# Kernel tuning notes

Hardware: AMD Instinct MI355X
Metric: run time of the kernel (lower is better)

The kernel has to match this reference:

```python
import jax, jax.numpy as jnp
import numpy as np
from math import factorial as _fact

# ---- sizes / hyperparams (match init_kwargs) ----
N_NODES, N_EDGES = 8192, 131072
C, H, NRAD, NUM_LAYERS = 64, 64, 8, 2
R_MAX, AVG_NN = 5.0, 16.0
LS = (0, 1, 2)  # irreps degrees carried by node features and edge SH

# ---- real-basis Clebsch-Gordan coefficients (computed once in numpy) ----
def _cg_scalar(j1, m1, j2, m2, j3, m3):
    if m1 + m2 != m3:
        return 0.0
    pre = ((2*j3+1) * _fact(j1+j2-j3) * _fact(j1-j2+j3) * _fact(-j1+j2+j3)
           / _fact(j1+j2+j3+1)) ** 0.5
    pre *= (_fact(j1+m1)*_fact(j1-m1)*_fact(j2+m2)*_fact(j2-m2)
            * _fact(j3+m3)*_fact(j3-m3)) ** 0.5
    s = 0.0
    for k in range(max(0, j2-j3-m1, j1+m2-j3), min(j1+j2-j3, j1-m1, j2+m2)+1):
        s += (-1)**k / (_fact(k)*_fact(j1+j2-j3-k)*_fact(j1-m1-k)
                        * _fact(j2+m2-k)*_fact(j3-j2+m1+k)*_fact(j3-j1-m2+k))
    return pre * s

def _U_real(l):
    # unitary: Y_real = U @ Y_complex, components ordered m=-l..l
    U = np.zeros((2*l+1, 2*l+1), dtype=complex)
    s2 = 2 ** -0.5
    for m in range(-l, l+1):
        if m > 0:
            U[m+l, m+l] = (-1)**m * s2
            U[m+l, -m+l] = s2
        elif m == 0:
            U[l, l] = 1.0
        else:
            U[m+l, m+l] = 1j*s2
            U[m+l, -m+l] = -1j*(-1)**(-m)*s2
    return U

def _real_cg(l1, l2, l3):
    Cc = np.zeros((2*l1+1, 2*l2+1, 2*l3+1))
    for i1, m1 in enumerate(range(-l1, l1+1)):
        for i2, m2 in enumerate(range(-l2, l2+1)):
            m3 = m1 + m2
            if abs(m3) <= l3:
                Cc[i1, i2, m3+l3] = _cg_scalar(l1, m1, l2, m2, l3, m3)
    U1, U2, U3 = _U_real(l1), _U_real(l2), _U_real(l3)
    W = np.einsum('ia,jb,kc,abc->ijk', U1.conj(), U2.conj(), U3, Cc.astype(complex))
    W = W.real if np.linalg.norm(W.real) >= np.linalg.norm(W.imag) else W.imag
    W = W / np.linalg.norm(W) * (2*l3+1) ** 0.5  # component-style normalization
    return jnp.asarray(W, dtype=jnp.float32)

PATHS = [(l1, l2, l3) for l1 in LS for l2 in LS for l3 in LS
         if abs(l1 - l2) <= l3 <= l1 + l2]  # 15 tensor-product paths
CGS = [_real_cg(*p) for p in PATHS]
N_PATHS = len(PATHS)


def _sph(u):
    # real spherical harmonics of unit vectors, l=0,1,2, m=-l..l ordering
    x, y, z = u[:, 0], u[:, 1], u[:, 2]
    sh0 = jnp.ones((u.shape[0], 1), u.dtype)
    sh1 = jnp.sqrt(3.0) * jnp.stack([y, z, x], axis=-1)
    sh2 = jnp.stack([jnp.sqrt(15.0)*x*y, jnp.sqrt(15.0)*y*z,
                     jnp.sqrt(5.0)/2*(3*z*z - 1.0),
                     jnp.sqrt(15.0)*x*z, jnp.sqrt(15.0)/2*(x*x - y*y)], axis=-1)
    return (sh0, sh1, sh2)


def _forward(positions, embed, w_proj, mlp_w1, mlp_b1, mlp_w2, mlp_b2, mlp_w3,
             lin_self, gate_w, gate_b, species, senders, receivers):
    n = positions.shape[0]
    rel = (positions[receivers] - positions[senders]) / R_MAX  # [E,3]
    d = jnp.linalg.norm(rel, axis=-1)                          # [E]
    u = rel / jnp.maximum(d, 1e-6)[:, None]
    sh = _sph(u)
    freqs = jnp.arange(1, NRAD + 1, dtype=positions.dtype)
    xr = jnp.clip(d, 1e-4, 1.0)[:, None]
    basis = jnp.sqrt(2.0) * jnp.sin(freqs * jnp.pi * xr) / xr  # Bessel [E,NRAD]
    cut = 0.5 * (jnp.cos(jnp.pi * jnp.clip(d, 0.0, 1.0)) + 1.0)  # smooth cutoff

    # initial species embedding -> scalar (0e) features; l>0 start at zero
    x0 = embed[species] @ w_proj                                # [N,C]
    feats = [x0[:, :, None],
             jnp.zeros((n, C, 3), x0.dtype),
             jnp.zeros((n, C, 5), x0.dtype)]

    inv_sqrt_nn = 1.0 / jnp.sqrt(jnp.asarray(AVG_NN, x0.dtype))
    for i in range(NUM_LAYERS):
        # radial MLP -> per-path, per-channel edge weights
        h = jax.nn.silu(basis @ mlp_w1[i] + mlp_b1[i])
        h = jax.nn.silu(h @ mlp_w2[i] + mlp_b2[i])
        w = (h @ mlp_w3[i]).reshape(-1, N_PATHS, C) * cut[:, None, None]
        xg = [feats[l][senders] for l in LS]                    # edge gather
        msgs = [0.0, 0.0, 0.0]
        for p, (l1, l2, l3) in enumerate(PATHS):
            m = jnp.einsum('eci,ej,ijk->eck', xg[l1], sh[l2], CGS[p])
            msgs[l3] = msgs[l3] + m * w[:, p, :, None]
        agg = [jax.ops.segment_sum(msgs[l], receivers, num_segments=n) * inv_sqrt_nn
               for l in LS]
        # self-interaction linears + gated nonlinearity + skip
        y = [jnp.einsum('ncm,cd->ndm', agg[l], lin_self[i, l]) for l in LS]
        feats[0] = feats[0] + jax.nn.silu(y[0])
        g_in = feats[0][:, :, 0]                                # [N,C] scalars
        for l in (1, 2):
            g = jax.nn.sigmoid(g_in @ gate_w[i, l-1] + gate_b[i, l-1])
            feats[l] = feats[l] + g[:, :, None] * y[l]

    # alpha = 0.5 ** l per irrep, then flatten to [N, C*(1+3+5)]
    return jnp.concatenate([(feats[l] * (0.5 ** l)).reshape(n, -1) for l in LS],
                           axis=-1)


def setup_inputs() -> dict:
    key = jax.random.key(0)
    ks = jax.random.split(key, 12)
    f32 = jnp.float32
    return {
        'positions': jax.random.normal(ks[0], (N_NODES, 3), f32),
        'species': jax.random.randint(ks[1], (N_NODES,), 0, 5),
        'senders': jax.random.randint(ks[2], (N_EDGES,), 0, N_NODES),
        'receivers': jax.random.randint(ks[3], (N_EDGES,), 0, N_NODES),
        'embed': jax.random.normal(ks[4], (5, 32), f32),
        'w_proj': jax.random.normal(ks[5], (32, C), f32) / jnp.sqrt(32.0),
        'mlp_w1': jax.random.normal(ks[6], (NUM_LAYERS, NRAD, H), f32) / jnp.sqrt(float(NRAD)),
        'mlp_b1': jnp.zeros((NUM_LAYERS, H), f32),
        'mlp_w2': jax.random.normal(ks[7], (NUM_LAYERS, H, H), f32) / jnp.sqrt(float(H)),
        'mlp_b2': jnp.zeros((NUM_LAYERS, H), f32),
        'mlp_w3': jax.random.normal(ks[8], (NUM_LAYERS, H, N_PATHS * C), f32) / jnp.sqrt(float(H)),
        'lin_self': jax.random.normal(ks[9], (NUM_LAYERS, 3, C, C), f32) / jnp.sqrt(float(C)),
        'gate_w': jax.random.normal(ks[10], (NUM_LAYERS, 2, C, C), f32) / jnp.sqrt(float(C)),
        'gate_b': jnp.zeros((NUM_LAYERS, 2, C), f32),
    }


def reference(positions, species, senders, receivers, embed, w_proj, mlp_w1,
              mlp_b1, mlp_w2, mlp_b2, mlp_w3, lin_self, gate_w, gate_b):
    return _forward(positions, embed, w_proj, mlp_w1, mlp_b1, mlp_w2, mlp_b2,
                    mlp_w3, lin_self, gate_w, gate_b, species, senders, receivers)
```

## Files before the change

### kernel.cpp

```cpp
#include <hip/hip_runtime.h>
#include <cmath>
#include <algorithm>

#define N_NODES 8192
#define N_EDGES 131072
#define NPATHS 15
#define FPN 576
#define NODE_BLK 8
#define NB_S 2
#define SWROW 968

typedef unsigned short ushortx;
typedef unsigned int uintx;
typedef short short8 __attribute__((ext_vector_type(8)));
typedef float f32x4 __attribute__((ext_vector_type(4)));

constexpr int PL1[NPATHS] = {0,0,0,1,1,1,1,1,1,2,2,2,2,2,2};
constexpr int PL2[NPATHS] = {0,1,2,0,1,1,1,2,2,0,1,1,2,2,2};
constexpr int PL3[NPATHS] = {0,1,2,1,0,1,2,1,2,2,1,2,0,1,2};
constexpr int CGOFF[NPATHS] = {0,1,10,35,44,53,80,125,170,245,270,315,390,415,490};
constexpr int CGTOT = 615;
constexpr int BOFF[3] = {0,1,4};

struct CGTable { float v[CGTOT]; };

constexpr double cfact(int n){ double r=1.0; for (int i=2;i<=n;++i) r*=i; return r; }
constexpr double csqrt(double x){
  if (x <= 0.0) return 0.0;
  double g = x < 1.0 ? 1.0 : x, p = 0.0;
  while (g != p){ p = g; g = 0.5*(g + x/g); }
  return g;
}
constexpr int cmax2(int a,int b){ return a>b?a:b; }
constexpr int cmin2(int a,int b){ return a<b?a:b; }

constexpr double cg_scalar_c(int j1,int m1,int j2,int m2,int j3,int m3){
  if (m1+m2 != m3) return 0.0;
  double pre = csqrt((2.0*j3+1.0)*cfact(j1+j2-j3)*cfact(j1-j2+j3)*cfact(-j1+j2+j3)/cfact(j1+j2+j3+1));
  pre *= csqrt(cfact(j1+m1)*cfact(j1-m1)*cfact(j2+m2)*cfact(j2-m2)*cfact(j3+m3)*cfact(j3-m3));
  double s = 0.0;
  int kmin = cmax2(0, cmax2(j2-j3-m1, j1+m2-j3));
  int kmax = cmin2(j1+j2-j3, cmin2(j1-m1, j2+m2));
  for (int k=kmin;k<=kmax;++k){
    double t = 1.0/(cfact(k)*cfact(j1+j2-j3-k)*cfact(j1-m1-k)*cfact(j2+m2-k)*cfact(j3-j2+m1+k)*cfact(j3-j1-m2+k));
    s += (k&1) ? -t : t;
  }
  return pre*s;
}

struct C2c { double re, im; };
constexpr C2c Uelem(int l, int a, int b){
  const double s2 = csqrt(0.5);
  const int m = a - l;
  C2c z{0.0, 0.0};
  if (m > 0){
    if (b ==  m+l) z = {((m&1)?-1.0:1.0)*s2, 0.0};
    else if (b == -m+l) z = {s2, 0.0};
  } else if (m == 0){
    if (b == l) z = {1.0, 0.0};
  } else {
    if (b ==  m+l) z = {0.0, s2};
    else if (b == -m+l) z = {0.0, -((((-m)&1))?-1.0:1.0)*s2};
  }
  return z;
}

constexpr CGTable build_cg(){
  CGTable t{};
  for (int p=0;p<NPATHS;++p){
    const int l1=PL1[p], l2=PL2[p], l3=PL3[p];
    const int n1=2*l1+1, n2=2*l2+1, n3=2*l3+1;
    double Cc[5][5][5] = {};
    for (int i1=0;i1<n1;++i1) for (int i2=0;i2<n2;++i2){
      int m1=i1-l1, m2=i2-l2, m3=m1+m2;
      if (m3 >= -l3 && m3 <= l3) Cc[i1][i2][m3+l3] = cg_scalar_c(l1,m1,l2,m2,l3,m3);
    }
    double Wre[5][5][5]={}, Wim[5][5][5]={};
    for (int i=0;i<n1;++i) for (int j=0;j<n2;++j) for (int k=0;k<n3;++k){
      double are=0.0, aim=0.0;
      for (int a=0;a<n1;++a) for (int b=0;b<n2;++b){
        int m3 = (a-l1)+(b-l2);
        if (m3 < -l3 || m3 > l3) continue;
        double cv = Cc[a][b][m3+l3];
        if (cv == 0.0) continue;
        C2c u1 = Uelem(l1,i,a);  u1.im = -u1.im;
        C2c u2 = Uelem(l2,j,b);  u2.im = -u2.im;
        C2c u3 = Uelem(l3,k,m3+l3);
        C2c u12{u1.re*u2.re - u1.im*u2.im, u1.re*u2.im + u1.im*u2.re};
        C2c tt {u12.re*u3.re - u12.im*u3.im, u12.re*u3.im + u12.im*u3.re};
        are += tt.re*cv; aim += tt.im*cv;
      }
      Wre[i][j][k]=are; Wim[i][j][k]=aim;
    }
    double nr=0.0, ni=0.0;
    for (int i=0;i<n1;++i) for (int j=0;j<n2;++j) for (int k=0;k<n3;++k){
      nr += Wre[i][j][k]*Wre[i][j][k]; ni += Wim[i][j][k]*Wim[i][j][k];
    }
    const bool useRe = csqrt(nr) >= csqrt(ni);
    const double nrm = csqrt(useRe ? nr : ni);
    const double scale = csqrt((double)n3) / nrm;
    for (int i=0;i<n1;++i) for (int j=0;j<n2;++j) for (int k=0;k<n3;++k)
      t.v[CGOFF[p] + (i*n2+j)*n3 + k] =
        (float)((useRe ? Wre[i][j][k] : Wim[i][j][k]) * scale);
  }
  return t;
}

inline constexpr CGTable CGC = build_cg();

__device__ __forceinline__ float siluf(float x){ return x / (1.0f + expf(-x)); }
__device__ __forceinline__ float sigmf(float x){ return 1.0f / (1.0f + expf(-x)); }
__device__ __forceinline__ ushortx f2b(float f){
  uintx u = __float_as_uint(f);
  u += 0x7fffu + ((u >> 16) & 1u);
  return (ushortx)(u >> 16);
}
__device__ __forceinline__ float b2f(ushortx b){ return __uint_as_float(((uintx)b) << 16); }
__device__ __forceinline__ float blo(uintx u){ return __uint_as_float(u << 16); }
__device__ __forceinline__ float bhi(uintx u){ return __uint_as_float(u & 0xffff0000u); }

template<int L1, int L2, int P0, int NP>
__device__ __forceinline__ void tp_combo(const float* __restrict__ X,
                                         const float* __restrict__ S,
                                         const float* __restrict__ w,
                                         float* __restrict__ m)
{
  #pragma unroll
  for (int i=0;i<2*L1+1;++i){
    #pragma unroll
    for (int j=0;j<2*L2+1;++j){
      const float xs = X[BOFF[L1]+i] * S[BOFF[L2]+j];
      #pragma unroll
      for (int pp=0;pp<NP;++pp){
        const int p  = P0 + pp;
        const int l3 = PL3[p];
        const int n3 = 2*l3+1;
        const float t = w[p] * xs;
        #pragma unroll
        for (int k=0;k<n3;++k){
          const float c = CGC.v[CGOFF[p] + (i*(2*L2+1)+j)*n3 + k];
          if (c != 0.0f) m[BOFF[l3]+k] = fmaf(c, t, m[BOFF[l3]+k]);
        }
      }
    }
  }
}

__global__ __launch_bounds__(64) void k_init(const int* __restrict__ species,
    const float* __restrict__ embed, const float* __restrict__ wproj,
    float* __restrict__ feats)
{
  const int n = blockIdx.x, c = threadIdx.x;
  const int sp = species[n];
  float acc = 0.f;
  #pragma unroll
  for (int q=0;q<32;++q) acc += embed[sp*32+q]*wproj[q*64+c];
  feats[n*FPN + c] = acc;
  #pragma unroll
  for (int r=1;r<9;++r) feats[n*FPN + r*64 + c] = 0.f;
}

__global__ __launch_bounds__(64) void k_out_t(const float* __restrict__ feats,
                                              float* __restrict__ out)
{
  const int n = blockIdx.x, c = threadIdx.x;
  const float* f = feats + (size_t)n*FPN;
  float* o = out + (size_t)n*FPN;
  o[c] = f[c];
  #pragma unroll
  for (int mm=0;mm<3;++mm) o[64 + c*3 + mm] = f[(1+mm)*64 + c] * 0.5f;
  #pragma unroll
  for (int mm=0;mm<5;++mm) o[256 + c*5 + mm] = f[(4+mm)*64 + c] * 0.25f;
}

__global__ __launch_bounds__(256) void k_hist(const int* __restrict__ receivers,
                                              int* __restrict__ cnt)
{
  int e = blockIdx.x*256 + threadIdx.x;
  atomicAdd(&cnt[receivers[e]], 1);
}

__global__ __launch_bounds__(1024) void k_scan(const int* __restrict__ cnt,
    int* __restrict__ row_start, int* __restrict__ cursor)
{
  __shared__ int part[1024];
  const int t = threadIdx.x;
  int loc[8];
  #pragma unroll
  for (int i=0;i<8;++i) loc[i] = cnt[t*8+i];
  int sum = 0;
  #pragma unroll
  for (int i=0;i<8;++i) sum += loc[i];
  part[t] = sum;
  __syncthreads();
  for (int off=1; off<1024; off<<=1){
    int x = (t >= off) ? part[t-off] : 0;
    __syncthreads();
    part[t] += x;
    __syncthreads();
  }
  int run = (t > 0) ? part[t-1] : 0;
  #pragma unroll
  for (int i=0;i<8;++i){
    row_start[t*8+i] = run;
    cursor[t*8+i]    = run;
    run += loc[i];
  }
  if (t == 1023) row_start[8192] = run;
}

__global__ __launch_bounds__(256) void k_scatter(const int* __restrict__ receivers,
    int* __restrict__ cursor, int* __restrict__ perm)
{
  int e = blockIdx.x*256 + threadIdx.x;
  int r = receivers[e];
  int pos = atomicAdd(&cursor[r], 1);
  perm[pos] = e;
}

__global__ __launch_bounds__(256) void k_geom(const float* __restrict__ pos,
    const int* __restrict__ senders, const int* __restrict__ receivers,
    const int* __restrict__ perm,
    float* __restrict__ sh8s, float* __restrict__ d_s,
    int* __restrict__ send_s, int* __restrict__ recv_s)
{
  const int i = blockIdx.x*256 + threadIdx.x;
  const int e = perm[i];
  const int s = senders[e], r = receivers[e];
  send_s[i] = s;
  recv_s[i] = r;
  float rx = (pos[r*3+0] - pos[s*3+0]) * 0.2f;
  float ry = (pos[r*3+1] - pos[s*3+1]) * 0.2f;
  float rz = (pos[r*3+2] - pos[s*3+2]) * 0.2f;
  float d  = sqrtf(rx*rx + ry*ry + rz*rz);
  d_s[i] = d;
  float iv = 1.0f / fmaxf(d, 1e-6f);
  float x = rx*iv, y = ry*iv, z = rz*iv;
  const float s3   = 1.7320508075688772f;
  const float s15  = 3.8729833462074170f;
  const float s5h  = 1.1180339887498949f;
  const float s15h = 1.9364916731037085f;
  sh8s[i*8+0] = s3*y;
  sh8s[i*8+1] = s3*z;
  sh8s[i*8+2] = s3*x;
  sh8s[i*8+3] = s15*x*y;
  sh8s[i*8+4] = s15*y*z;
  sh8s[i*8+5] = s5h*(3.f*z*z - 1.f);
  sh8s[i*8+6] = s15*x*z;
  sh8s[i*8+7] = s15h*(x*x - y*y);
}

__global__ __launch_bounds__(256) void k_mlp(
    const float* __restrict__ d_s,
    const float* __restrict__ w1, const float* __restrict__ b1,
    const float* __restrict__ w2, const float* __restrict__ b2,
    ushortx* __restrict__ h2p)
{
  __shared__ float s_w2[4096];
  __shared__ float s_h1[4*64];
  const int tid = threadIdx.x, wv = tid>>6, lane = tid&63;
  const float PI = 3.14159265358979323846f;
  for (int i=tid;i<4096;i+=256) s_w2[i] = w2[i];
  __syncthreads();
  #pragma unroll
  for (int ee=0; ee<2; ++ee){
    const int i = blockIdx.x*8 + wv*2 + ee;
    const float d = d_s[i];
    float xr = fminf(fmaxf(d, 1e-4f), 1.0f);
    float ixr = 1.0f/xr;
    float acc = b1[lane];
    #pragma unroll
    for (int q=0;q<8;++q){
      float bs = 1.4142135623730951f * sinf((float)(q+1)*PI*xr) * ixr;
      acc = fmaf(bs, w1[q*64+lane], acc);
    }
    s_h1[wv*64+lane] = siluf(acc);
    __syncthreads();
    float acc2 = b2[lane];
    #pragma unroll
    for (int k=0;k<64;++k) acc2 = fmaf(s_h1[wv*64+k], s_w2[k*64+lane], acc2);
    float dc = fminf(fmaxf(d, 0.f), 1.f);
    float cut = 0.5f*(cosf(PI*dc) + 1.f);
    float h2 = siluf(acc2) * cut * 0.25f;
    h2p[(size_t)i*64+lane] = f2b(h2);
    __syncthreads();
  }
}

__global__ __launch_bounds__(256) void k_w3t(const float* __restrict__ w3,
                                             ushortx* __restrict__ w3t)
{
  int g = blockIdx.x*256 + threadIdx.x;
  int n = g >> 6, k = g & 63;
  w3t[g] = f2b(w3[k*960 + n]);
}

__global__ __launch_bounds__(256) void k_gemmW(
    const ushortx* __restrict__ h2p, const ushortx* __restrict__ w3t,
    const int* __restrict__ rowst, int n0c, int n1c,
    ushortx* __restrict__ wgt, int capE)
{
  __shared__ ushortx s_c[16*1024];
  const int eBeg = rowst[n0c], eEnd = rowst[n1c];
  const int e0 = eBeg + blockIdx.x*16;
  if (e0 >= eEnd) return;
  const int tid = threadIdx.x, wv = tid >> 6, lane = tid & 63;
  const int q = lane >> 4, mrow = lane & 15;

  int ia = e0 + mrow;
  if (ia >= eEnd) ia = eEnd - 1;
  short8 a0 = *(const short8*)&h2p[(size_t)ia*64 +      q*8];
  short8 a1 = *(const short8*)&h2p[(size_t)ia*64 + 32 + q*8];

  #pragma unroll
  for (int nt=0; nt<15; ++nt){
    const int col = wv*240 + nt*16 + mrow;
    short8 b0 = *(const short8*)&w3t[(size_t)col*64 +      q*8];
    short8 b1 = *(const short8*)&w3t[(size_t)col*64 + 32 + q*8];
    f32x4 acc = {0.f,0.f,0.f,0.f};
    acc = __builtin_amdgcn_mfma_f32_16x16x32_bf16(a0, b0, acc, 0, 0, 0);
    acc = __builtin_amdgcn_mfma_f32_16x16x32_bf16(a1, b1, acc, 0, 0, 0);
    const int p = col >> 6, ch = col & 63;
    #pragma unroll
    for (int r=0;r<4;++r)
      s_c[(q*4+r)*1024 + ch*16 + p] = f2b(acc[r]);
  }
  __syncthreads();

  const uint4* sc4 = (const uint4*)s_c;
  uint4* wg4 = (uint4*)wgt;
  #pragma unroll
  for (int it=0; it<8; ++it){
    const int j = it*256 + tid;
    const int er = j >> 7, c16 = j & 127;
    const int erow = e0 + er, rel = erow - eBeg;
    if (erow < eEnd && rel < capE)
      wg4[(size_t)rel*128 + c16] = sc4[j];
  }
}

__global__ __launch_bounds__(256) void k_aggS(
    const float* __restrict__ featsIn, float* __restrict__ featsOut,
    const ushortx* __restrict__ wgt, const float* __restrict__ sh8s,
    const int* __restrict__ send_s, const int* __restrict__ recv_s,
    const int* __restrict__ rowst, int n0c,
    const float* __restrict__ lin, const float* __restrict__ gw,
    const float* __restrict__ gb, int capE)
{
  __shared__ float s_agg[NB_S*FPN];

  const int tid  = threadIdx.x;
  const int wv   = tid >> 6;
  const int lane = tid & 63;
  const int n0   = n0c + blockIdx.x * NB_S;
  const int beg  = rowst[n0];
  const int end  = rowst[n0 + NB_S];
  const int eBeg = rowst[n0c];

  for (int k = tid; k < NB_S*FPN; k += 256) s_agg[k] = 0.f;
  __syncthreads();

  for (int i = beg + wv; i < end; i += 4){
    const int s  = send_s[i];
    const int rl = recv_s[i] - n0;
    const float* fb = featsIn + (size_t)s*FPN;
    float X[9];
    #pragma unroll
    for (int r=0;r<9;++r) X[r] = fb[r*64 + lane];
    float S[9];
    S[0] = 1.f;
    #pragma unroll
    for (int jj=0;jj<8;++jj) S[1+jj] = sh8s[(size_t)i*8+jj];
    const int rel = i - eBeg;
    const uint4* wp = (const uint4*)(wgt + (size_t)(rel < capE ? rel : capE-1)*1024 + lane*16);
    uint4 ua = wp[0], ub = wp[1];
    float w[NPATHS];
    w[0]=blo(ua.x);  w[1]=bhi(ua.x);  w[2]=blo(ua.y);  w[3]=bhi(ua.y);
    w[4]=blo(ua.z);  w[5]=bhi(ua.z);  w[6]=blo(ua.w);  w[7]=bhi(ua.w);
    w[8]=blo(ub.x);  w[9]=bhi(ub.x);  w[10]=blo(ub.y); w[11]=bhi(ub.y);
    w[12]=blo(ub.z); w[13]=bhi(ub.z); w[14]=blo(ub.w);
    float m[9];
    #pragma unroll
    for (int k=0;k<9;++k) m[k] = 0.f;

    tp_combo<0,0, 0,1>(X,S,w,m);
    tp_combo<0,1, 1,1>(X,S,w,m);
    tp_combo<0,2, 2,1>(X,S,w,m);
    tp_combo<1,0, 3,1>(X,S,w,m);
    tp_combo<1,1, 4,3>(X,S,w,m);
    tp_combo<1,2, 7,2>(X,S,w,m);
    tp_combo<2,0, 9,1>(X,S,w,m);
    tp_combo<2,1,10,2>(X,S,w,m);
    tp_combo<2,2,12,3>(X,S,w,m);

    float* ab = s_agg + rl*FPN;
    #pragma unroll
    for (int r=0;r<9;++r) atomicAdd(&ab[r*64 + lane], m[r]);
  }
  __syncthreads();

  if (wv < NB_S){
    const int ln = wv;
    const int n  = n0 + ln;
    const float* ag = s_agg + ln*FPN;
    float y[9];
    #pragma unroll
    for (int j=0;j<9;++j) y[j] = 0.f;
    for (int c=0;c<64;++c){
      float l0 = lin[          c*64 + lane];
      float l1 = lin[4096    + c*64 + lane];
      float l2 = lin[8192    + c*64 + lane];
      y[0] = fmaf(ag[c], l0, y[0]);
      #pragma unroll
      for (int mm=0;mm<3;++mm) y[1+mm] = fmaf(ag[(1+mm)*64 + c], l1, y[1+mm]);
      #pragma unroll
      for (int mm=0;mm<5;++mm) y[4+mm] = fmaf(ag[(4+mm)*64 + c], l2, y[4+mm]);
    }
    const size_t base = (size_t)n*FPN;
    float f0 = featsIn[base + lane] + siluf(y[0]);
    featsOut[base + lane] = f0;
    float a1 = gb[lane], a2 = gb[64 + lane];
    for (int c=0;c<64;++c){
      float fc = __shfl(f0, c);
      a1 = fmaf(fc, gw[        c*64 + lane], a1);
      a2 = fmaf(fc, gw[4096 +  c*64 + lane], a2);
    }
    float g1 = sigmf(a1), g2 = sigmf(a2);
    #pragma unroll
    for (int mm=0;mm<3;++mm)
      featsOut[base + (1+mm)*64 + lane] = featsIn[base + (1+mm)*64 + lane] + g1*y[1+mm];
    #pragma unroll
    for (int mm=0;mm<5;++mm)
      featsOut[base + (4+mm)*64 + lane] = featsIn[base + (4+mm)*64 + lane] + g2*y[4+mm];
  }
}

__global__ __launch_bounds__(256) void k_aggmm(
    const float* __restrict__ featsIn, float* __restrict__ featsOut,
    const ushortx* __restrict__ h2p, const ushortx* __restrict__ w3t,
    const float* __restrict__ sh8s, const int* __restrict__ send_s,
    const int* __restrict__ recv_s, const int* __restrict__ rowst,
    const float* __restrict__ lin, const float* __restrict__ gw,
    const float* __restrict__ gb)
{
  __shared__ float   s_agg[NODE_BLK*FPN];
  __shared__ ushortx s_w[16*SWROW];
  __shared__ ushortx s_a[16*72];

  const int tid  = threadIdx.x;
  const int wv   = tid >> 6;
  const int lane = tid & 63;
  const int n0   = blockIdx.x * NODE_BLK;
  const int beg  = rowst[n0];
  const int end  = rowst[n0 + NODE_BLK];

  for (int k = tid; k < NODE_BLK*FPN; k += 256) s_agg[k] = 0.f;
  __syncthreads();

  const int q = lane >> 4, mrow = lane & 15;

  for (int ebeg = beg; ebeg < end; ebeg += 16){
    {
      int er = tid >> 4, seg = tid & 15;
      int i = ebeg + er;
      if (i >= end) i = end - 1;
      *(uint2*)&s_a[er*72 + seg*4] =
        *(const uint2*)&h2p[(size_t)i*64 + seg*4];
    }
    __syncthreads();

    short8 a0 = *(const short8*)&s_a[mrow*72 +      q*8];
    short8 a1 = *(const short8*)&s_a[mrow*72 + 32 + q*8];
    #pragma unroll
    for (int nt=0; nt<15; ++nt){
      const int col = wv*240 + nt*16 + mrow;
      short8 b0 = *(const short8*)&w3t[(size_t)col*64 +      q*8];
      short8 b1 = *(const short8*)&w3t[(size_t)col*64 + 32 + q*8];
      f32x4 acc = {0.f,0.f,0.f,0.f};
      acc = __builtin_amdgcn_mfma_f32_16x16x32_bf16(a0, b0, acc, 0, 0, 0);
      acc = __builtin_amdgcn_mfma_f32_16x16x32_bf16(a1, b1, acc, 0, 0, 0);
      #pragma unroll
      for (int r=0;r<4;++r)
        s_w[(q*4+r)*SWROW + col] = f2b(acc[r]);
    }
    __syncthreads();

    #pragma unroll
    for (int ee=0; ee<4; ++ee){
      const int slot = wv*4 + ee;
      const int i = ebeg + slot;
      if (i < end){
        const int s  = send_s[i];
        const int rl = recv_s[i] - n0;
        const float* fb = featsIn + (size_t)s*FPN;
        float X[9];
        #pragma unroll
        for (int r=0;r<9;++r) X[r] = fb[r*64 + lane];
        float S[9];
        S[0] = 1.f;
        #pragma unroll
        for (int jj=0;jj<8;++jj) S[1+jj] = sh8s[(size_t)i*8+jj];
        float w[NPATHS];
        #pragma unroll
        for (int p=0;p<NPATHS;++p) w[p] = b2f(s_w[slot*SWROW + p*64 + lane]);
        float m[9];
        #pragma unroll
        for (int k=0;k<9;++k) m[k] = 0.f;

        tp_combo<0,0, 0,1>(X,S,w,m);
        tp_combo<0,1, 1,1>(X,S,w,m);
        tp_combo<0,2, 2,1>(X,S,w,m);
        tp_combo<1,0, 3,1>(X,S,w,m);
        tp_combo<1,1, 4,3>(X,S,w,m);
        tp_combo<1,2, 7,2>(X,S,w,m);
        tp_combo<2,0, 9,1>(X,S,w,m);
        tp_combo<2,1,10,2>(X,S,w,m);
        tp_combo<2,2,12,3>(X,S,w,m);

        float* ab = s_agg + rl*FPN;
        #pragma unroll
        for (int r=0;r<9;++r) atomicAdd(&ab[r*64 + lane], m[r]);
      }
    }
    __syncthreads();
  }

  #pragma unroll
  for (int k=0;k<2;++k){
    const int ln = wv*2 + k;
    const int n  = n0 + ln;
    const float* ag = s_agg + ln*FPN;
    float y[9];
    #pragma unroll
    for (int j=0;j<9;++j) y[j] = 0.f;
    for (int c=0;c<64;++c){
      float l0 = lin[          c*64 + lane];
      float l1 = lin[4096    + c*64 + lane];
      float l2 = lin[8192    + c*64 + lane];
      y[0] = fmaf(ag[c], l0, y[0]);
      #pragma unroll
      for (int mm=0;mm<3;++mm) y[1+mm] = fmaf(ag[(1+mm)*64 + c], l1, y[1+mm]);
      #pragma unroll
      for (int mm=0;mm<5;++mm) y[4+mm] = fmaf(ag[(4+mm)*64 + c], l2, y[4+mm]);
    }
    const size_t base = (size_t)n*FPN;
    float f0 = featsIn[base + lane] + siluf(y[0]);
    featsOut[base + lane] = f0;
    float a1 = gb[lane], a2 = gb[64 + lane];
    for (int c=0;c<64;++c){
      float fc = __shfl(f0, c);
      a1 = fmaf(fc, gw[        c*64 + lane], a1);
      a2 = fmaf(fc, gw[4096 +  c*64 + lane], a2);
    }
    float g1 = sigmf(a1), g2 = sigmf(a2);
    #pragma unroll
    for (int mm=0;mm<3;++mm)
      featsOut[base + (1+mm)*64 + lane] = featsIn[base + (1+mm)*64 + lane] + g1*y[1+mm];
    #pragma unroll
    for (int mm=0;mm<5;++mm)
      featsOut[base + (4+mm)*64 + lane] = featsIn[base + (4+mm)*64 + lane] + g2*y[4+mm];
  }
}

__global__ __launch_bounds__(64) void k_init_fb(const int* __restrict__ species,
    const float* __restrict__ embed, const float* __restrict__ wproj,
    float* __restrict__ feats)
{
  const int n = blockIdx.x, c = threadIdx.x;
  const int sp = species[n];
  float acc = 0.f;
  #pragma unroll
  for (int q=0;q<32;++q) acc += embed[sp*32+q]*wproj[q*64+c];
  feats[n*FPN + c] = acc;
  #pragma unroll
  for (int j=0;j<8;++j) feats[n*FPN + 64 + j*64 + c] = 0.f;
}

__global__ __launch_bounds__(256) void k_out_fb(const float* __restrict__ feats,
                                                float* __restrict__ out)
{
  const int n = blockIdx.x;
  for (int j = threadIdx.x; j < FPN; j += 256){
    float sc = (j < 64) ? 1.0f : ((j < 256) ? 0.5f : 0.25f);
    out[n*FPN + j] = feats[n*FPN + j] * sc;
  }
}

__global__ __launch_bounds__(256) void k_edge_fb(
    const float* __restrict__ pos,
    const int* __restrict__ senders, const int* __restrict__ receivers,
    const float* __restrict__ w1, const float* __restrict__ b1,
    const float* __restrict__ w2, const float* __restrict__ b2,
    const float* __restrict__ w3,
    const float* __restrict__ feats, float* __restrict__ agg,
    const CGTable cg)
{
  __shared__ float s_h1[16*64];
  __shared__ float s_h2[16*64];
  __shared__ float s_w3[8*960];
  __shared__ float s_sh[16][8];
  __shared__ float s_cut[16];

  const int tid  = threadIdx.x;
  const int wave = tid >> 6;
  const int lane = tid & 63;
  const int ebase = blockIdx.x * 16;
  const float PI = 3.14159265358979323846f;

  #pragma unroll
  for (int ee=0; ee<4; ++ee){
    const int slot = wave*4 + ee;
    const int e = ebase + slot;
    const int s = senders[e], r = receivers[e];
    float rx = (pos[r*3+0] - pos[s*3+0]) * 0.2f;
    float ry = (pos[r*3+1] - pos[s*3+1]) * 0.2f;
    float rz = (pos[r*3+2] - pos[s*3+2]) * 0.2f;
    float d  = sqrtf(rx*rx + ry*ry + rz*rz);
    float iv = 1.0f / fmaxf(d, 1e-6f);
    float x = rx*iv, y = ry*iv, z = rz*iv;
    if (lane == 0){
      const float s3   = 1.7320508075688772f;
      const float s15  = 3.8729833462074170f;
      const float s5h  = 1.1180339887498949f;
      const float s15h = 1.9364916731037085f;
      s_sh[slot][0] = s3*y;  s_sh[slot][1] = s3*z;  s_sh[slot][2] = s3*x;
      s_sh[slot][3] = s15*x*y; s_sh[slot][4] = s15*y*z;
      s_sh[slot][5] = s5h*(3.f*z*z - 1.f);
      s_sh[slot][6] = s15*x*z; s_sh[slot][7] = s15h*(x*x - y*y);
      float dc = fminf(fmaxf(d, 0.f), 1.f);
      s_cut[slot] = 0.5f*(cosf(PI*dc) + 1.f);
    }
    float xr = fminf(fmaxf(d, 1e-4f), 1.0f);
    float ixr = 1.0f/xr;
    float acc = b1[lane];
    #pragma unroll
    for (int q=0;q<8;++q)
      acc += 1.4142135623730951f * sinf((float)(q+1)*PI*xr) * ixr * w1[q*64 + lane];
    s_h1[slot*64 + lane] = siluf(acc);
  }
  __syncthreads();
  #pragma unroll
  for (int ee=0; ee<4; ++ee){
    const int slot = wave*4 + ee;
    float acc = b2[lane];
    #pragma unroll
    for (int k=0;k<64;++k) acc += s_h1[slot*64+k] * w2[k*64+lane];
    s_h2[slot*64+lane] = siluf(acc);
  }
  __syncthreads();

  float wgt[NPATHS][4];
  #pragma unroll
  for (int p=0;p<NPATHS;++p){ wgt[p][0]=wgt[p][1]=wgt[p][2]=wgt[p][3]=0.f; }
  for (int kc=0;kc<8;++kc){
    #pragma unroll
    for (int rr=0;rr<8;++rr){
      #pragma unroll
      for (int jj=0;jj<4;++jj){
        int col = jj*256 + tid;
        if (col < 960) s_w3[rr*960+col] = w3[(kc*8+rr)*960+col];
      }
    }
    __syncthreads();
    #pragma unroll
    for (int kk=0;kk<8;++kk){
      float h2v[4];
      #pragma unroll
      for (int ee=0;ee<4;++ee) h2v[ee] = s_h2[(wave*4+ee)*64 + kc*8+kk];
      #pragma unroll
      for (int p=0;p<NPATHS;++p){
        float wv = s_w3[kk*960 + p*64 + lane];
        #pragma unroll
        for (int ee=0;ee<4;++ee) wgt[p][ee] = fmaf(h2v[ee], wv, wgt[p][ee]);
      }
    }
    __syncthreads();
  }
  #pragma unroll
  for (int ee=0;ee<4;++ee){
    float f = s_cut[wave*4+ee] * 0.25f;
    #pragma unroll
    for (int p=0;p<NPATHS;++p) wgt[p][ee] *= f;
  }
  #pragma unroll
  for (int ee=0;ee<4;++ee){
    const int slot = wave*4 + ee;
    const int e = ebase + slot;
    const int s = senders[e];
    const int r = receivers[e];
    const int sb = s*FPN;
    float X[9], S[9], msg[9];
    X[0] = feats[sb + lane];
    #pragma unroll
    for (int mm=0;mm<3;++mm) X[1+mm] = feats[sb + 64  + lane*3 + mm];
    #pragma unroll
    for (int mm=0;mm<5;++mm) X[4+mm] = feats[sb + 256 + lane*5 + mm];
    S[0] = 1.f;
    #pragma unroll
    for (int j=0;j<8;++j) S[1+j] = s_sh[slot][j];
    #pragma unroll
    for (int k=0;k<9;++k) msg[k] = 0.f;
    #pragma unroll
    for (int p=0;p<NPATHS;++p){
      const int l1=PL1[p], l2=PL2[p], l3=PL3[p];
      const int n2=2*l2+1, n3=2*l3+1;
      const float wp = wgt[p][ee];
      #pragma unroll
      for (int i=0;i<2*l1+1;++i){
        #pragma unroll
        for (int j=0;j<n2;++j){
          float t = wp * X[BOFF[l1]+i] * S[BOFF[l2]+j];
          #pragma unroll
          for (int k=0;k<n3;++k)
            msg[BOFF[l3]+k] = fmaf(cg.v[CGOFF[p] + (i*n2+j)*n3 + k], t, msg[BOFF[l3]+k]);
        }
      }
    }
    const int rb = r*FPN;
    unsafeAtomicAdd(&agg[rb + lane], msg[0]);
    #pragma unroll
    for (int mm=0;mm<3;++mm) unsafeAtomicAdd(&agg[rb + 64  + lane*3 + mm], msg[1+mm]);
    #pragma unroll
    for (int mm=0;mm<5;++mm) unsafeAtomicAdd(&agg[rb + 256 + lane*5 + mm], msg[4+mm]);
  }
}

__global__ __launch_bounds__(64) void k_node_fb(
    float* __restrict__ feats, const float* __restrict__ agg,
    const float* __restrict__ lin, const float* __restrict__ gw,
    const float* __restrict__ gb)
{
  __shared__ float sf0[64];
  const int n = blockIdx.x, d = threadIdx.x;
  const int base = n*FPN;
  float y[9];
  #pragma unroll
  for (int k=0;k<9;++k) y[k]=0.f;
  for (int c=0;c<64;++c){
    float l0 = lin[          c*64 + d];
    float l1 = lin[4096    + c*64 + d];
    float l2 = lin[8192    + c*64 + d];
    y[0] = fmaf(agg[base + c], l0, y[0]);
    #pragma unroll
    for (int mm=0;mm<3;++mm) y[1+mm] = fmaf(agg[base + 64  + c*3 + mm], l1, y[1+mm]);
    #pragma unroll
    for (int mm=0;mm<5;++mm) y[4+mm] = fmaf(agg[base + 256 + c*5 + mm], l2, y[4+mm]);
  }
  float f0 = feats[base + d] + siluf(y[0]);
  feats[base + d] = f0;
  sf0[d] = f0;
  __syncthreads();
  {
    float acc = gb[d];
    for (int c=0;c<64;++c) acc = fmaf(sf0[c], gw[c*64 + d], acc);
    float g = sigmf(acc);
    #pragma unroll
    for (int mm=0;mm<3;++mm) feats[base + 64 + d*3 + mm] += g*y[1+mm];
  }
  {
    float acc = gb[64 + d];
    for (int c=0;c<64;++c) acc = fmaf(sf0[c], gw[4096 + c*64 + d], acc);
    float g = sigmf(acc);
    #pragma unroll
    for (int mm=0;mm<5;++mm) feats[base + 256 + d*5 + mm] += g*y[4+mm];
  }
}

extern "C" void kernel_launch(void* const* d_in, const int* in_sizes, int n_in,
                              void* d_out, int out_size, void* d_ws, size_t ws_size,
                              hipStream_t stream)
{
  const float* pos      = (const float*)d_in[0];
  const int*   species  = (const int*)  d_in[1];
  const int*   senders  = (const int*)  d_in[2];
  const int*   receivers= (const int*)  d_in[3];
  const float* embed    = (const float*)d_in[4];
  const float* wproj    = (const float*)d_in[5];
  const float* w1       = (const float*)d_in[6];
  const float* b1       = (const float*)d_in[7];
  const float* w2       = (const float*)d_in[8];
  const float* b2       = (const float*)d_in[9];
  const float* w3       = (const float*)d_in[10];
  const float* lin      = (const float*)d_in[11];
  const float* gw       = (const float*)d_in[12];
  const float* gb       = (const float*)d_in[13];

  char* p = (char*)d_ws;
  size_t off = 0;
  auto alloc = [&](size_t bytes)->char*{
    char* r = p + off;
    off += (bytes + 255) & ~(size_t)255;
    return r;
  };
  float*   featsA  = (float*)  alloc((size_t)N_NODES*FPN*4);
  float*   featsB  = (float*)  alloc((size_t)N_NODES*FPN*4);
  int*     cnt     = (int*)    alloc(N_NODES*4);
  int*     cursor  = (int*)    alloc(N_NODES*4);
  int*     rowst   = (int*)    alloc((N_NODES+1)*4);
  int*     perm    = (int*)    alloc((size_t)N_EDGES*4);
  int*     send_s  = (int*)    alloc((size_t)N_EDGES*4);
  int*     recv_s  = (int*)    alloc((size_t)N_EDGES*4);
  float*   d_sArr  = (float*)  alloc((size_t)N_EDGES*4);
  float*   sh8s    = (float*)  alloc((size_t)N_EDGES*8*4);
  ushortx* h2p     = (ushortx*)alloc((size_t)N_EDGES*64*2);
  ushortx* w3t     = (ushortx*)alloc((size_t)960*64*2);
  const size_t need_common = off;

  int strideN = 0;
  size_t capE = 0;
  const int strides[4] = {8192, 4096, 2048, 1024};
  for (int t=0; t<4; ++t){
    size_t cap = (size_t)strides[t]*16 + ((strides[t] == 8192) ? 0 : 2048);
    if (need_common + cap*2048 <= ws_size){ strideN = strides[t]; capE = cap; break; }
  }

  if (need_common <= ws_size){
    hipMemsetAsync(cnt, 0, N_NODES*4, stream);
    hipLaunchKernelGGL(k_hist,    dim3(N_EDGES/256), dim3(256), 0, stream, receivers, cnt);
    hipLaunchKernelGGL(k_scan,    dim3(1), dim3(1024), 0, stream, cnt, rowst, cursor);
    hipLaunchKernelGGL(k_scatter, dim3(N_EDGES/256), dim3(256), 0, stream, receivers, cursor, perm);
    hipLaunchKernelGGL(k_geom,    dim3(N_EDGES/256), dim3(256), 0, stream,
                       pos, senders, receivers, perm, sh8s, d_sArr, send_s, recv_s);
    hipLaunchKernelGGL(k_init,    dim3(N_NODES), dim3(64), 0, stream,
                       species, embed, wproj, featsA);
    if (strideN > 0){
      ushortx* wgt = (ushortx*)alloc(capE*2048);
      const int chunks = N_NODES / strideN;
      for (int L=0; L<2; ++L){
        const float* fin  = (L == 0) ? featsA : featsB;
        float*       fout = (L == 0) ? featsB : featsA;
        hipLaunchKernelGGL(k_mlp,  dim3(N_EDGES/8), dim3(256), 0, stream,
                           d_sArr, w1 + L*512, b1 + L*64, w2 + L*4096, b2 + L*64, h2p);
        hipLaunchKernelGGL(k_w3t,  dim3(240), dim3(256), 0, stream, w3 + (size_t)L*61440, w3t);
        for (int c=0; c<chunks; ++c){
          const int n0c = c*strideN, n1c = n0c + strideN;
          hipLaunchKernelGGL(k_gemmW, dim3((unsigned)(capE/16)), dim3(256), 0, stream,
                             h2p, w3t, rowst, n0c, n1c, wgt, (int)capE);
          hipLaunchKernelGGL(k_aggS, dim3(strideN/NB_S), dim3(256), 0, stream,
                             fin, fout, wgt, sh8s, send_s, recv_s, rowst, n0c,
                             lin + L*3*64*64, gw + L*2*64*64, gb + L*2*64, (int)capE);
        }
      }
    } else {
      for (int L=0; L<2; ++L){
        const float* fin  = (L == 0) ? featsA : featsB;
        float*       fout = (L == 0) ? featsB : featsA;
        hipLaunchKernelGGL(k_mlp,  dim3(N_EDGES/8), dim3(256), 0, stream,
                           d_sArr, w1 + L*512, b1 + L*64, w2 + L*4096, b2 + L*64, h2p);
        hipLaunchKernelGGL(k_w3t,  dim3(240), dim3(256), 0, stream, w3 + (size_t)L*61440, w3t);
        hipLaunchKernelGGL(k_aggmm, dim3(N_NODES/NODE_BLK), dim3(256), 0, stream,
                           fin, fout, h2p, w3t, sh8s, send_s, recv_s, rowst,
                           lin + L*3*64*64, gw + L*2*64*64, gb + L*2*64);
      }
    }
    hipLaunchKernelGGL(k_out_t, dim3(N_NODES), dim3(64), 0, stream, featsA, (float*)d_out);
  } else {
    float* feats = (float*)d_ws;
    float* agg   = feats + (size_t)N_NODES*FPN;
    hipLaunchKernelGGL(k_init_fb, dim3(N_NODES), dim3(64), 0, stream,
                       species, embed, wproj, feats);
    for (int L=0; L<2; ++L){
      hipMemsetAsync(agg, 0, (size_t)N_NODES*FPN*sizeof(float), stream);
      hipLaunchKernelGGL(k_edge_fb, dim3(N_EDGES/16), dim3(256), 0, stream,
                         pos, senders, receivers,
                         w1 + L*512, b1 + L*64, w2 + L*4096, b2 + L*64,
                         w3 + (size_t)L*61440, feats, agg, CGC);
      hipLaunchKernelGGL(k_node_fb, dim3(N_NODES), dim3(64), 0, stream,
                         feats, agg, lin + L*3*64*64, gw + L*2*64*64, gb + L*2*64);
    }
    hipLaunchKernelGGL(k_out_fb, dim3(N_NODES), dim3(256), 0, stream, feats, (float*)d_out);
  }
}
```

Measured before the change: 1.544 ms.

## Gather sender features from a packed bf16 per-channel copy, two edges per wave

Node kernels now also write a bf16 copy of the node features, laid out per channel as 10 contiguous halfwords. The edge aggregation then gathers each sender's 9 irrep components with one 16-byte load plus one scalar load, instead of 9 strided fp32 loads. The aggregation loop also handles two edges per wave iteration to raise memory-level parallelism. The largest chunk stride is dropped to make room for the extra buffers, which may add a gemmW/aggS launch pair per layer, and the message inputs lose precision because they are now bf16.

```diff
diff --git a/kernel.cpp b/kernel.cpp
--- a/kernel.cpp
+++ b/kernel.cpp
@@ -6,6 +6,7 @@
 #define N_EDGES 131072
 #define NPATHS 15
 #define FPN 576
+#define FGW 10
 #define NODE_BLK 8
 #define NB_S 2
 #define SWROW 968
@@ -146,9 +147,25 @@
   }
 }
 
+__device__ __forceinline__ void tp_all(const float* __restrict__ X,
+                                       const float* __restrict__ S,
+                                       const float* __restrict__ w,
+                                       float* __restrict__ m)
+{
+  tp_combo<0,0, 0,1>(X,S,w,m);
+  tp_combo<0,1, 1,1>(X,S,w,m);
+  tp_combo<0,2, 2,1>(X,S,w,m);
+  tp_combo<1,0, 3,1>(X,S,w,m);
+  tp_combo<1,1, 4,3>(X,S,w,m);
+  tp_combo<1,2, 7,2>(X,S,w,m);
+  tp_combo<2,0, 9,1>(X,S,w,m);
+  tp_combo<2,1,10,2>(X,S,w,m);
+  tp_combo<2,2,12,3>(X,S,w,m);
+}
+
 __global__ __launch_bounds__(64) void k_init(const int* __restrict__ species,
     const float* __restrict__ embed, const float* __restrict__ wproj,
-    float* __restrict__ feats)
+    float* __restrict__ feats, ushortx* __restrict__ featsG)
 {
   const int n = blockIdx.x, c = threadIdx.x;
   const int sp = species[n];
@@ -158,6 +175,10 @@
   feats[n*FPN + c] = acc;
   #pragma unroll
   for (int r=1;r<9;++r) feats[n*FPN + r*64 + c] = 0.f;
+  ushortx* g = featsG + (size_t)n*64*FGW + c*FGW;
+  g[0] = f2b(acc);
+  #pragma unroll
+  for (int r=1;r<FGW;++r) g[r] = 0;
 }
 
 __global__ __launch_bounds__(64) void k_out_t(const float* __restrict__ feats,
@@ -341,6 +362,7 @@
 
 __global__ __launch_bounds__(256) void k_aggS(
     const float* __restrict__ featsIn, float* __restrict__ featsOut,
+    const ushortx* __restrict__ gin, ushortx* __restrict__ gout,
     const ushortx* __restrict__ wgt, const float* __restrict__ sh8s,
     const int* __restrict__ send_s, const int* __restrict__ recv_s,
     const int* __restrict__ rowst, int n0c,
@@ -360,49 +382,70 @@
   for (int k = tid; k < NB_S*FPN; k += 256) s_agg[k] = 0.f;
   __syncthreads();
 
-  for (int i = beg + wv; i < end; i += 4){
-    const int s  = send_s[i];
-    const int rl = recv_s[i] - n0;
-    const float* fb = featsIn + (size_t)s*FPN;
-    float X[9];
-    #pragma unroll
-    for (int r=0;r<9;++r) X[r] = fb[r*64 + lane];
-    float S[9];
-    S[0] = 1.f;
-    #pragma unroll
-    for (int jj=0;jj<8;++jj) S[1+jj] = sh8s[(size_t)i*8+jj];
-    const int rel = i - eBeg;
-    const uint4* wp = (const uint4*)(wgt + (size_t)(rel < capE ? rel : capE-1)*1024 + lane*16);
-    uint4 ua = wp[0], ub = wp[1];
-    float w[NPATHS];
-    w[0]=blo(ua.x);  w[1]=bhi(ua.x);  w[2]=blo(ua.y);  w[3]=bhi(ua.y);
-    w[4]=blo(ua.z);  w[5]=bhi(ua.z);  w[6]=blo(ua.w);  w[7]=bhi(ua.w);
-    w[8]=blo(ub.x);  w[9]=bhi(ub.x);  w[10]=blo(ub.y); w[11]=bhi(ub.y);
-    w[12]=blo(ub.z); w[13]=bhi(ub.z); w[14]=blo(ub.w);
-    float m[9];
-    #pragma unroll
-    for (int k=0;k<9;++k) m[k] = 0.f;
-
-    tp_combo<0,0, 0,1>(X,S,w,m);
-    tp_combo<0,1, 1,1>(X,S,w,m);
-    tp_combo<0,2, 2,1>(X,S,w,m);
-    tp_combo<1,0, 3,1>(X,S,w,m);
-    tp_combo<1,1, 4,3>(X,S,w,m);
-    tp_combo<1,2, 7,2>(X,S,w,m);
-    tp_combo<2,0, 9,1>(X,S,w,m);
-    tp_combo<2,1,10,2>(X,S,w,m);
-    tp_combo<2,2,12,3>(X,S,w,m);
-
-    float* ab = s_agg + rl*FPN;
-    #pragma unroll
-    for (int r=0;r<9;++r) atomicAdd(&ab[r*64 + lane], m[r]);
+  for (int i = beg + wv; i < end; i += 8){
+    const int iB   = i + 4;
+    const bool hasB = iB < end;
+    const int iBc  = hasB ? iB : i;
+
+    const int sA  = send_s[i],   sB  = send_s[iBc];
+    const int rlA = recv_s[i] - n0, rlB = recv_s[iBc] - n0;
+    const ushortx* fA = gin + (size_t)sA*64*FGW + lane*FGW;
+    const ushortx* fB = gin + (size_t)sB*64*FGW + lane*FGW;
+    uint4 xA = *(const uint4*)fA;  ushortx xA8 = fA[8];
+    uint4 xB = *(const uint4*)fB;  ushortx xB8 = fB[8];
+    const int relA = i   - eBeg;
+    const int relB = iBc - eBeg;
+    const uint4* wpA = (const uint4*)(wgt + (size_t)(relA < capE ? relA : capE-1)*1024 + lane*16);
+    const uint4* wpB = (const uint4*)(wgt + (size_t)(relB < capE ? relB : capE-1)*1024 + lane*16);
+    uint4 uaA = wpA[0], ubA = wpA[1];
+    uint4 uaB = wpB[0], ubB = wpB[1];
+    float SA[9], SB[9];
+    SA[0] = 1.f; SB[0] = 1.f;
+    #pragma unroll
+    for (int j=0;j<8;++j){ SA[1+j] = sh8s[(size_t)i*8+j]; SB[1+j] = sh8s[(size_t)iBc*8+j]; }
+
+    {
+      float X[9];
+      X[0]=blo(xA.x); X[1]=bhi(xA.x); X[2]=blo(xA.y); X[3]=bhi(xA.y);
+      X[4]=blo(xA.z); X[5]=bhi(xA.z); X[6]=blo(xA.w); X[7]=bhi(xA.w);
+      X[8]=b2f(xA8);
+      float w[NPATHS];
+      w[0]=blo(uaA.x);  w[1]=bhi(uaA.x);  w[2]=blo(uaA.y);  w[3]=bhi(uaA.y);
+      w[4]=blo(uaA.z);  w[5]=bhi(uaA.z);  w[6]=blo(uaA.w);  w[7]=bhi(uaA.w);
+      w[8]=blo(ubA.x);  w[9]=bhi(ubA.x);  w[10]=blo(ubA.y); w[11]=bhi(ubA.y);
+      w[12]=blo(ubA.z); w[13]=bhi(ubA.z); w[14]=blo(ubA.w);
+      float m[9];
+      #pragma unroll
+      for (int k=0;k<9;++k) m[k] = 0.f;
+      tp_all(X, SA, w, m);
+      float* ab = s_agg + rlA*FPN;
+      #pragma unroll
+      for (int r=0;r<9;++r) atomicAdd(&ab[r*64 + lane], m[r]);
+    }
+    if (hasB){
+      float X[9];
+      X[0]=blo(xB.x); X[1]=bhi(xB.x); X[2]=blo(xB.y); X[3]=bhi(xB.y);
+      X[4]=blo(xB.z); X[5]=bhi(xB.z); X[6]=blo(xB.w); X[7]=bhi(xB.w);
+      X[8]=b2f(xB8);
+      float w[NPATHS];
+      w[0]=blo(uaB.x);  w[1]=bhi(uaB.x);  w[2]=blo(uaB.y);  w[3]=bhi(uaB.y);
+      w[4]=blo(uaB.z);  w[5]=bhi(uaB.z);  w[6]=blo(uaB.w);  w[7]=bhi(uaB.w);
+      w[8]=blo(ubB.x);  w[9]=bhi(ubB.x);  w[10]=blo(ubB.y); w[11]=bhi(ubB.y);
+      w[12]=blo(ubB.z); w[13]=bhi(ubB.z); w[14]=blo(ubB.w);
+      float m[9];
+      #pragma unroll
+      for (int k=0;k<9;++k) m[k] = 0.f;
+      tp_all(X, SB, w, m);
+      float* ab = s_agg + rlB*FPN;
+      #pragma unroll
+      for (int r=0;r<9;++r) atomicAdd(&ab[r*64 + lane], m[r]);
+    }
   }
   __syncthreads();
 
   if (wv < NB_S){
-    const int ln = wv;
-    const int n  = n0 + ln;
-    const float* ag = s_agg + ln*FPN;
+    const int n  = n0 + wv;
+    const float* ag = s_agg + wv*FPN;
     float y[9];
     #pragma unroll
     for (int j=0;j<9;++j) y[j] = 0.f;
@@ -417,8 +460,10 @@
       for (int mm=0;mm<5;++mm) y[4+mm] = fmaf(ag[(4+mm)*64 + c], l2, y[4+mm]);
     }
     const size_t base = (size_t)n*FPN;
+    ushortx* g = gout + (size_t)n*64*FGW + lane*FGW;
     float f0 = featsIn[base + lane] + siluf(y[0]);
     featsOut[base + lane] = f0;
+    g[0] = f2b(f0);
     float a1 = gb[lane], a2 = gb[64 + lane];
     for (int c=0;c<64;++c){
       float fc = __shfl(f0, c);
@@ -427,11 +472,17 @@
     }
     float g1 = sigmf(a1), g2 = sigmf(a2);
     #pragma unroll
-    for (int mm=0;mm<3;++mm)
-      featsOut[base + (1+mm)*64 + lane] = featsIn[base + (1+mm)*64 + lane] + g1*y[1+mm];
-    #pragma unroll
-    for (int mm=0;mm<5;++mm)
-      featsOut[base + (4+mm)*64 + lane] = featsIn[base + (4+mm)*64 + lane] + g2*y[4+mm];
+    for (int mm=0;mm<3;++mm){
+      float v = featsIn[base + (1+mm)*64 + lane] + g1*y[1+mm];
+      featsOut[base + (1+mm)*64 + lane] = v;
+      g[1+mm] = f2b(v);
+    }
+    #pragma unroll
+    for (int mm=0;mm<5;++mm){
+      float v = featsIn[base + (4+mm)*64 + lane] + g2*y[4+mm];
+      featsOut[base + (4+mm)*64 + lane] = v;
+      g[4+mm] = f2b(v);
+    }
   }
 }
 
@@ -506,17 +557,7 @@
         float m[9];
         #pragma unroll
         for (int k=0;k<9;++k) m[k] = 0.f;
-
-        tp_combo<0,0, 0,1>(X,S,w,m);
-        tp_combo<0,1, 1,1>(X,S,w,m);
-        tp_combo<0,2, 2,1>(X,S,w,m);
-        tp_combo<1,0, 3,1>(X,S,w,m);
-        tp_combo<1,1, 4,3>(X,S,w,m);
-        tp_combo<1,2, 7,2>(X,S,w,m);
-        tp_combo<2,0, 9,1>(X,S,w,m);
-        tp_combo<2,1,10,2>(X,S,w,m);
-        tp_combo<2,2,12,3>(X,S,w,m);
-
+        tp_all(X, S, w, m);
         float* ab = s_agg + rl*FPN;
         #pragma unroll
         for (int r=0;r<9;++r) atomicAdd(&ab[r*64 + lane], m[r]);
@@ -804,17 +845,22 @@
   float*   sh8s    = (float*)  alloc((size_t)N_EDGES*8*4);
   ushortx* h2p     = (ushortx*)alloc((size_t)N_EDGES*64*2);
   ushortx* w3t     = (ushortx*)alloc((size_t)960*64*2);
-  const size_t need_common = off;
+  const size_t need_base = off;
+
+  ushortx* featsGA = (ushortx*)alloc((size_t)N_NODES*64*FGW*2);
+  ushortx* featsGB = (ushortx*)alloc((size_t)N_NODES*64*FGW*2);
+  const size_t need_split_base = off;
 
   int strideN = 0;
   size_t capE = 0;
-  const int strides[4] = {8192, 4096, 2048, 1024};
-  for (int t=0; t<4; ++t){
-    size_t cap = (size_t)strides[t]*16 + ((strides[t] == 8192) ? 0 : 2048);
-    if (need_common + cap*2048 <= ws_size){ strideN = strides[t]; capE = cap; break; }
-  }
-
-  if (need_common <= ws_size){
+  const int strides[3] = {4096, 2048, 1024};
+  for (int t=0; t<3; ++t){
+    size_t cap = (size_t)strides[t]*16 + 2048;
+    if (need_split_base + cap*2048 <= ws_size){ strideN = strides[t]; capE = cap; break; }
+  }
+
+  if (strideN > 0){
+    ushortx* wgt = (ushortx*)alloc(capE*2048);
     hipMemsetAsync(cnt, 0, N_NODES*4, stream);
     hipLaunchKernelGGL(k_hist,    dim3(N_EDGES/256), dim3(256), 0, stream, receivers, cnt);
     hipLaunchKernelGGL(k_scan,    dim3(1), dim3(1024), 0, stream, cnt, rowst, cursor);
@@ -822,36 +868,46 @@
     hipLaunchKernelGGL(k_geom,    dim3(N_EDGES/256), dim3(256), 0, stream,
                        pos, senders, receivers, perm, sh8s, d_sArr, send_s, recv_s);
     hipLaunchKernelGGL(k_init,    dim3(N_NODES), dim3(64), 0, stream,
+                       species, embed, wproj, featsA, featsGA);
+    const int chunks = N_NODES / strideN;
+    for (int L=0; L<2; ++L){
+      const float* fin  = (L == 0) ? featsA : featsB;
+      float*       fout = (L == 0) ? featsB : featsA;
+      const ushortx* gin  = (L == 0) ? featsGA : featsGB;
+      ushortx*       gout = (L == 0) ? featsGB : featsGA;
+      hipLaunchKernelGGL(k_mlp,  dim3(N_EDGES/8), dim3(256), 0, stream,
+                         d_sArr, w1 + L*512, b1 + L*64, w2 + L*4096, b2 + L*64, h2p);
+      hipLaunchKernelGGL(k_w3t,  dim3(240), dim3(256), 0, stream, w3 + (size_t)L*61440, w3t);
+      for (int c=0; c<chunks; ++c){
+        const int n0c = c*strideN, n1c = n0c + strideN;
+        hipLaunchKernelGGL(k_gemmW, dim3((unsigned)(capE/16)), dim3(256), 0, stream,
+                           h2p, w3t, rowst, n0c, n1c, wgt, (int)capE);
+        hipLaunchKernelGGL(k_aggS, dim3(strideN/NB_S), dim3(256), 0, stream,
+                           fin, fout, gin, gout, wgt, sh8s, send_s, recv_s, rowst, n0c,
+                           lin + L*3*64*64, gw + L*2*64*64, gb + L*2*64, (int)capE);
+      }
+    }
+    hipLaunchKernelGGL(k_out_t, dim3(N_NODES), dim3(64), 0, stream, featsA, (float*)d_out);
+  } else if (need_base <= ws_size){
+    hipMemsetAsync(cnt, 0, N_NODES*4, stream);
+    hipLaunchKernelGGL(k_hist,    dim3(N_EDGES/256), dim3(256), 0, stream, receivers, cnt);
+    hipLaunchKernelGGL(k_scan,    dim3(1), dim3(1024), 0, stream, cnt, rowst, cursor);
+    hipLaunchKernelGGL(k_scatter, dim3(N_EDGES/256), dim3(256), 0, stream, receivers, cursor, perm);
+    hipLaunchKernelGGL(k_geom,    dim3(N_EDGES/256), dim3(256), 0, stream,
+                       pos, senders, receivers, perm, sh8s, d_sArr, send_s, recv_s);
+    hipLaunchKernelGGL(k_init_fb, dim3(N_NODES), dim3(64), 0, stream,
                        species, embed, wproj, featsA);
-    if (strideN > 0){
-      ushortx* wgt = (ushortx*)alloc(capE*2048);
-      const int chunks = N_NODES / strideN;
-      for (int L=0; L<2; ++L){
-        const float* fin  = (L == 0) ? featsA : featsB;
-        float*       fout = (L == 0) ? featsB : featsA;
-        hipLaunchKernelGGL(k_mlp,  dim3(N_EDGES/8), dim3(256), 0, stream,
-                           d_sArr, w1 + L*512, b1 + L*64, w2 + L*4096, b2 + L*64, h2p);
-        hipLaunchKernelGGL(k_w3t,  dim3(240), dim3(256), 0, stream, w3 + (size_t)L*61440, w3t);
-        for (int c=0; c<chunks; ++c){
-          const int n0c = c*strideN, n1c = n0c + strideN;
-          hipLaunchKernelGGL(k_gemmW, dim3((unsigned)(capE/16)), dim3(256), 0, stream,
-                             h2p, w3t, rowst, n0c, n1c, wgt, (int)capE);
-          hipLaunchKernelGGL(k_aggS, dim3(strideN/NB_S), dim3(256), 0, stream,
-                             fin, fout, wgt, sh8s, send_s, recv_s, rowst, n0c,
-                             lin + L*3*64*64, gw + L*2*64*64, gb + L*2*64, (int)capE);
-        }
-      }
-    } else {
-      for (int L=0; L<2; ++L){
-        const float* fin  = (L == 0) ? featsA : featsB;
-        float*       fout = (L == 0) ? featsB : featsA;
-        hipLaunchKernelGGL(k_mlp,  dim3(N_EDGES/8), dim3(256), 0, stream,
-                           d_sArr, w1 + L*512, b1 + L*64, w2 + L*4096, b2 + L*64, h2p);
-        hipLaunchKernelGGL(k_w3t,  dim3(240), dim3(256), 0, stream, w3 + (size_t)L*61440, w3t);
-        hipLaunchKernelGGL(k_aggmm, dim3(N_NODES/NODE_BLK), dim3(256), 0, stream,
-                           fin, fout, h2p, w3t, sh8s, send_s, recv_s, rowst,
-                           lin + L*3*64*64, gw + L*2*64*64, gb + L*2*64);
-      }
+    hipLaunchKernelGGL(k_init,    dim3(N_NODES), dim3(64), 0, stream,
+                       species, embed, wproj, featsA, featsGA);
+    for (int L=0; L<2; ++L){
+      const float* fin  = (L == 0) ? featsA : featsB;
+      float*       fout = (L == 0) ? featsB : featsA;
+      hipLaunchKernelGGL(k_mlp,  dim3(N_EDGES/8), dim3(256), 0, stream,
+                         d_sArr, w1 + L*512, b1 + L*64, w2 + L*4096, b2 + L*64, h2p);
+      hipLaunchKernelGGL(k_w3t,  dim3(240), dim3(256), 0, stream, w3 + (size_t)L*61440, w3t);
+      hipLaunchKernelGGL(k_aggmm, dim3(N_NODES/NODE_BLK), dim3(256), 0, stream,
+                         fin, fout, h2p, w3t, sh8s, send_s, recv_s, rowst,
+                         lin + L*3*64*64, gw + L*2*64*64, gb + L*2*64);
     }
     hipLaunchKernelGGL(k_out_t, dim3(N_NODES), dim3(64), 0, stream, featsA, (float*)d_out);
   } else {
```

After: 1.554 ms. About the same (+0.6%).
